# Kernel tuning notes

Measured on AMD Instinct MI355X. Metric: run time of the kernel, lower is better.

## Reference

```python
import jax, jax.numpy as jnp
import numpy as np
import math

# Model/config constants (from LunarisCodexConfig defaults)
B, S, D = 4, 4096, 768
E = 8            # n_experts
TOP_K = 2
H = 2048         # SwiGLU hidden: multiple_of*ceil((2/3*4*768)/256)
CAP_F = 1.25     # capacity_factor
EPS = 1e-6       # RMSNorm eps
ALPHA = 1.0      # 1/sqrt(n_reasoning_steps), n_reasoning_steps=1


def setup_inputs() -> dict:
    key = jax.random.key(0)
    k0, k1, k2, k3 = jax.random.split(key, 4)
    x = jax.random.normal(k0, (B, S, D), jnp.float32)
    gate_w = jax.random.normal(k1, (E, D), jnp.float32) * 0.02          # router
    w13 = jax.random.normal(k2, (E, 2 * H, D), jnp.float32) * 0.02      # fused gate/up per expert
    w2 = jax.random.normal(k3, (E, D, H), jnp.float32) * 0.02           # down proj per expert
    norm_w = jnp.ones((E, D), jnp.float32)                              # per-expert RMSNorm weight
    return {"x": x, "gate_w": gate_w, "w13": w13, "w2": w2, "norm_w": norm_w}


def reference(x, gate_w, w13, w2, norm_w):
    Bx, Sx, Dx = x.shape
    N = Bx * Sx
    cap = int(math.ceil(CAP_F * TOP_K * N / E))
    xf = x.reshape(N, Dx)

    # ---- router in fp32, top-k gating with renormalized weights ----
    logits = xf.astype(jnp.float32) @ gate_w.T                 # [N, E]
    probs = jax.nn.softmax(logits, axis=-1)
    top_p, top_i = jax.lax.top_k(probs, TOP_K)                 # [N, K]
    w = top_p / jnp.sum(top_p, axis=-1, keepdims=True)         # [N, K]

    # ---- vectorized capacity-based dispatch (token-major, k-minor order) ----
    flat_e = top_i.reshape(-1)                                  # [N*K]
    onehot = jax.nn.one_hot(flat_e, E, dtype=jnp.int32)         # [N*K, E]
    pos = jnp.take_along_axis(jnp.cumsum(onehot, axis=0) - 1,
                              flat_e[:, None], axis=1)[:, 0]    # rank within expert
    keep = pos < cap                                            # capacity mask
    didx = flat_e * cap + jnp.minimum(pos, cap - 1)             # slot id in [0, E*cap)
    safe = jnp.where(keep, didx, E * cap)                       # dropped -> scratch row

    x_rep = jnp.repeat(xf, TOP_K, axis=0)                       # [N*K, D]
    buf = jnp.zeros((E * cap + 1, Dx), x.dtype).at[safe].set(x_rep)
    buf = buf[:-1].reshape(E, cap, Dx)                          # [E, C, D]

    z = 2.0 * buf
    z = z * jax.lax.rsqrt(jnp.mean(z * z, axis=-1, keepdims=True) + EPS)
    z = z * norm_w[:, None, :]
    gu = jnp.einsum('ecd,ehd->ech', z, w13)                     # [E, C, 2H]
    g, u = jnp.split(gu, 2, axis=-1)
    y = buf + ALPHA * jnp.einsum('ech,edh->ecd', jax.nn.silu(g) * u, w2)

    # ---- combine: gather back, weight, drop over-capacity slots ----
    y_tok = y.reshape(E * cap, Dx)[didx]                        # [N*K, D]
    cw = (w.reshape(-1) * keep.astype(w.dtype)).astype(x.dtype)
    out = (cw[:, None] * y_tok).reshape(N, TOP_K, Dx).sum(axis=1)
    return out.reshape(Bx, Sx, Dx)
```

## Files before the change

### kernel.cpp

```cpp
#include <hip/hip_runtime.h>
#include <hip/hip_bf16.h>
#include <stdint.h>


#define N_TOK 16384
#define D_    768
#define E_    8
#define H_    2048
#define CAP   5120
#define NK    (N_TOK * 2)
#define EPS_  1e-6f
#define LDE   72

typedef unsigned short u16;
typedef __attribute__((ext_vector_type(8))) __bf16 v8bf;
typedef __attribute__((ext_vector_type(4))) float  v4f;

typedef __attribute__((address_space(3))) unsigned int lds_u32;
typedef const __attribute__((address_space(1))) unsigned int glb_u32;

__device__ __forceinline__ void gload16(const void* g, void* lds) {
    __builtin_amdgcn_global_load_lds((glb_u32*)g, (lds_u32*)lds, 16, 0, 0);
}

__device__ __forceinline__ float bf2f(u16 u) {
    union { uint32_t i; float f; } v; v.i = ((uint32_t)u) << 16; return v.f;
}
__device__ __forceinline__ u16 f2bf(float f) {
    union { uint32_t i; float f; } v; v.f = f;
    uint32_t r = v.i + 0x7fffu + ((v.i >> 16) & 1u);
    return (u16)(r >> 16);
}

__global__ __launch_bounds__(256) void conv_bf16_kernel(
    const float* __restrict__ src, u16* __restrict__ dst, int n4)
{
    for (int i = blockIdx.x * 256 + threadIdx.x; i < n4; i += gridDim.x * 256) {
        float4 v = ((const float4*)src)[i];
        ushort4 o;
        o.x = f2bf(v.x); o.y = f2bf(v.y); o.z = f2bf(v.z); o.w = f2bf(v.w);
        ((ushort4*)dst)[i] = o;
    }
}

__global__ __launch_bounds__(256) void router_kernel(
    const float* __restrict__ x, const float* __restrict__ gate_w,
    int* __restrict__ routerEx, float* __restrict__ routerW)
{
    __shared__ float gw[E_ * D_];
    int t = threadIdx.x;
    for (int i = t; i < E_ * D_; i += 256) gw[i] = gate_w[i];
    __syncthreads();
    int wv = t >> 6, l = t & 63;
    int n = blockIdx.x * 4 + wv;
    const float* xr = x + (size_t)n * D_;
    float p[E_];
#pragma unroll
    for (int e = 0; e < E_; ++e) p[e] = 0.f;
#pragma unroll
    for (int j = 0; j < 12; ++j) {
        int d = l + 64 * j;
        float xv = xr[d];
#pragma unroll
        for (int e = 0; e < E_; ++e) p[e] += xv * gw[e * D_ + d];
    }
#pragma unroll
    for (int off = 32; off > 0; off >>= 1) {
#pragma unroll
        for (int e = 0; e < E_; ++e) p[e] += __shfl_xor(p[e], off, 64);
    }
    if (l == 0) {
        int e0 = 0; float m0 = p[0];
#pragma unroll
        for (int e = 1; e < E_; ++e) if (p[e] > m0) { m0 = p[e]; e0 = e; }
        int e1 = (e0 == 0) ? 1 : 0; float m1 = p[e1];
#pragma unroll
        for (int e = 0; e < E_; ++e) if (e != e0 && p[e] > m1) { m1 = p[e]; e1 = e; }
        float w0 = 1.f / (1.f + __expf(m1 - m0));
        routerEx[2 * n] = e0; routerEx[2 * n + 1] = e1;
        routerW[2 * n] = w0; routerW[2 * n + 1] = 1.f - w0;
    }
}

__global__ __launch_bounds__(256) void dispatch_kernel(
    const int* __restrict__ routerEx, int* __restrict__ tokenSlot,
    int* __restrict__ slotToken, int* __restrict__ cnt)
{
    __shared__ int hist[256 * E_];
    int t = threadIdx.x;
    int loc[E_];
#pragma unroll
    for (int e = 0; e < E_; ++e) loc[e] = 0;
    int base = t * (NK / 256);
    for (int j = 0; j < NK / 256; ++j) {
        int ev = routerEx[base + j];
#pragma unroll
        for (int e = 0; e < E_; ++e) loc[e] += (ev == e) ? 1 : 0;
    }
#pragma unroll
    for (int e = 0; e < E_; ++e) hist[t * E_ + e] = loc[e];
    __syncthreads();
    if (t < E_) {
        int run = 0;
        for (int tt = 0; tt < 256; ++tt) { int v = hist[tt * E_ + t]; hist[tt * E_ + t] = run; run += v; }
        cnt[t] = run;
    }
    __syncthreads();
    int off[E_];
#pragma unroll
    for (int e = 0; e < E_; ++e) off[e] = hist[t * E_ + e];
    for (int j = 0; j < NK / 256; ++j) {
        int i = base + j;
        int ev = routerEx[i];
        int pos = 0;
#pragma unroll
        for (int e = 0; e < E_; ++e) { if (ev == e) { pos = off[e]; off[e] = pos + 1; } }
        if (pos < CAP) {
            int s = ev * CAP + pos;
            tokenSlot[i] = s;
            slotToken[s] = i;
        } else {
            tokenSlot[i] = -1;
        }
    }
}

__global__ __launch_bounds__(256) void init_out_kernel(
    const float* __restrict__ x, const int* __restrict__ tokenSlot,
    const float* __restrict__ routerW, float* __restrict__ out)
{
    int g = blockIdx.x * 256 + threadIdx.x;
    int n = g / 96;
    int d0 = (g - n * 96) * 8;
    float w0 = (tokenSlot[2 * n] >= 0) ? routerW[2 * n] : 0.f;
    float w1 = (tokenSlot[2 * n + 1] >= 0) ? routerW[2 * n + 1] : 0.f;
    float ws = w0 + w1;
    const float* xr = x + (size_t)n * D_ + d0;
    float* orow = out + (size_t)n * D_ + d0;
    float4 a = *(const float4*)&xr[0];
    float4 b = *(const float4*)&xr[4];
    float4 oa, ob;
    oa.x = ws * a.x; oa.y = ws * a.y; oa.z = ws * a.z; oa.w = ws * a.w;
    ob.x = ws * b.x; ob.y = ws * b.y; ob.z = ws * b.z; ob.w = ws * b.w;
    *(float4*)&orow[0] = oa;
    *(float4*)&orow[4] = ob;
}

__global__ __launch_bounds__(256) void gather_norm_kernel(
    const float* __restrict__ x, const float* __restrict__ norm_w,
    const int* __restrict__ slotToken, const int* __restrict__ cnt,
    u16* __restrict__ zAll, size_t zStride, int eFixed)
{
    int e = eFixed + blockIdx.z;
    u16* zE = zAll + (size_t)blockIdx.z * zStride;
    int t = threadIdx.x, wv = t >> 6, l = t & 63;
    int pos = blockIdx.x * 4 + wv;
    int ce = min(cnt[e], CAP);
    u16* zr = zE + (size_t)pos * D_;
    if (pos >= ce) {
        ushort4 zz = { 0, 0, 0, 0 };
#pragma unroll
        for (int j = 0; j < 3; ++j) *(ushort4*)&zr[l * 4 + 256 * j] = zz;
        return;
    }
    int tok = slotToken[e * CAP + pos] >> 1;
    const float* xr = x + (size_t)tok * D_;
    float xv[12]; float ss = 0.f;
#pragma unroll
    for (int j = 0; j < 3; ++j) {
        float4 v4 = *(const float4*)&xr[l * 4 + 256 * j];
        xv[4 * j] = v4.x; xv[4 * j + 1] = v4.y; xv[4 * j + 2] = v4.z; xv[4 * j + 3] = v4.w;
        ss += v4.x * v4.x + v4.y * v4.y + v4.z * v4.z + v4.w * v4.w;
    }
#pragma unroll
    for (int off = 32; off > 0; off >>= 1) ss += __shfl_xor(ss, off, 64);
    float rs = rsqrtf(4.f * ss * (1.f / (float)D_) + EPS_);
    const float* nw = norm_w + e * D_;
#pragma unroll
    for (int j = 0; j < 3; ++j) {
        int d0 = l * 4 + 256 * j;
        float4 nv = *(const float4*)&nw[d0];
        ushort4 o;
        o.x = f2bf(2.f * xv[4 * j]     * rs * nv.x);
        o.y = f2bf(2.f * xv[4 * j + 1] * rs * nv.y);
        o.z = f2bf(2.f * xv[4 * j + 2] * rs * nv.z);
        o.w = f2bf(2.f * xv[4 * j + 3] * rs * nv.w);
        *(ushort4*)&zr[d0] = o;
    }
}

__global__ __launch_bounds__(256, 2) void gemm1_kernel(
    const u16* __restrict__ zAll, size_t zStride,
    const u16* __restrict__ w13All, size_t wStride,
    u16* __restrict__ actAll, size_t actStride,
    const int* __restrict__ cnt, int eFixed)
{
    int hw  = blockIdx.y * 32 + blockIdx.x;
    int xcd = hw & 7, cid = hw >> 3;
    int jn  = (xcd & 3) * 8 + (cid & 7);
    int rb  = (xcd >> 2) * 20 + (cid >> 3);
    int e   = eFixed + blockIdx.z;
    int ce  = min(cnt[e], CAP);
    if (rb * 128 >= ce) return;
    const u16* zE   = zAll   + (size_t)blockIdx.z * zStride;
    const u16* w13e = w13All + (size_t)blockIdx.z * wStride;
    u16*       actE = actAll + (size_t)blockIdx.z * actStride;

    __shared__ __align__(16) u16 smem[2 * 128 * 64];
    u16* As = smem;
    u16* Bs = smem + 128 * 64;

    int t = threadIdx.x, w = t >> 6, l = t & 63;
    int lr  = l >> 3;
    int lsw = ((l & 7) ^ lr) << 4;

    const char* aSrc = (const char*)zE
        + (size_t)(rb * 128 + w * 32 + lr) * (D_ * 2) + lsw;
    int rr0   = w * 32 + lr;
    int grow0 = (w < 2) ? (jn * 64 + rr0) : (H_ + jn * 64 + rr0 - 64);
    const char* bSrc = (const char*)w13e + (size_t)grow0 * (D_ * 2) + lsw;

    const v4f vzero = { 0.f, 0.f, 0.f, 0.f };
    v4f acc[2][8];
#pragma unroll
    for (int i = 0; i < 2; ++i)
#pragma unroll
        for (int j = 0; j < 8; ++j) acc[i][j] = vzero;

    int fr = l & 15;
    int sw = (l & 7) << 4;
    int fq = (l >> 4) << 4;

    for (int kb = 0; kb < D_ / 64; ++kb) {
        __syncthreads();
#pragma unroll
        for (int i = 0; i < 4; ++i) {
            gload16(aSrc + i * (8 * D_ * 2), &As[(w * 32 + i * 8) * 64]);
            gload16(bSrc + i * (8 * D_ * 2), &Bs[(w * 32 + i * 8) * 64]);
        }
        aSrc += 128; bSrc += 128;
        __syncthreads();
#pragma unroll
        for (int ks = 0; ks < 2; ++ks) {
            int kby = (ks * 64 + fq) ^ sw;
            v8bf a0 = *(const v8bf*)((const char*)As + (w * 32      + fr) * 128 + kby);
            v8bf a1 = *(const v8bf*)((const char*)As + (w * 32 + 16 + fr) * 128 + kby);
            v8bf bv[8];
#pragma unroll
            for (int ct = 0; ct < 8; ++ct)
                bv[ct] = *(const v8bf*)((const char*)Bs + (ct * 16 + fr) * 128 + kby);
#pragma unroll
            for (int ct = 0; ct < 8; ++ct) {
                acc[0][ct] = __builtin_amdgcn_mfma_f32_16x16x32_bf16(a0, bv[ct], acc[0][ct], 0, 0, 0);
                acc[1][ct] = __builtin_amdgcn_mfma_f32_16x16x32_bf16(a1, bv[ct], acc[1][ct], 0, 0, 0);
            }
        }
    }
    __syncthreads();
    u16* ep = smem;
    int colb = l & 15, rowq = (l >> 4) * 4;
#pragma unroll
    for (int rt = 0; rt < 2; ++rt) {
#pragma unroll
        for (int cg = 0; cg < 4; ++cg) {
            v4f g = acc[rt][cg], u = acc[rt][cg + 4];
#pragma unroll
            for (int r = 0; r < 4; ++r) {
                int rl = w * 32 + rt * 16 + rowq + r;
                float gv = g[r], uv = u[r];
                ep[rl * LDE + cg * 16 + colb] = f2bf(gv / (1.f + __expf(-gv)) * uv);
            }
        }
    }
    __syncthreads();
#pragma unroll
    for (int i = 0; i < 4; ++i) {
        int rl = (t >> 3) + 32 * i;
        int c0 = (t & 7) * 8;
        uint4 v = *(const uint4*)&ep[rl * LDE + c0];
        *(uint4*)&actE[(size_t)(rb * 128 + rl) * H_ + jn * 64 + c0] = v;
    }
}

template <bool WRITE_DELTA>
__global__ __launch_bounds__(256, 2) void gemm2_kernel(
    const u16* __restrict__ actAll, size_t actStride,
    const u16* __restrict__ w2All, size_t wStride,
    const int* __restrict__ slotToken, const float* __restrict__ routerW,
    float* __restrict__ out, u16* __restrict__ deltaAll, size_t deltaStride,
    const int* __restrict__ cnt, int eFixed)
{
    int hw  = blockIdx.y * 12 + blockIdx.x;
    int xcd = hw & 7, cid = hw >> 3;
    int jn  = cid % 12;
    int rb  = xcd * 5 + cid / 12;
    int e   = eFixed + blockIdx.z;
    int ce  = min(cnt[e], CAP);
    if (rb * 128 >= ce) return;
    const u16* actE = actAll + (size_t)blockIdx.z * actStride;
    const u16* w2e  = w2All  + (size_t)blockIdx.z * wStride;

    __shared__ __align__(16) u16 smem[128 * 64 + 64 * 64];
    u16* As = smem;
    u16* Bs = smem + 128 * 64;

    int t = threadIdx.x, w = t >> 6, l = t & 63;
    int lr  = l >> 3;
    int lsw = ((l & 7) ^ lr) << 4;

    const char* aSrc = (const char*)actE
        + (size_t)(rb * 128 + w * 32 + lr) * (H_ * 2) + lsw;
    const char* bSrc = (const char*)w2e
        + (size_t)(jn * 64 + w * 16 + lr) * (H_ * 2) + lsw;

    const v4f vzero = { 0.f, 0.f, 0.f, 0.f };
    v4f acc[2][4];
#pragma unroll
    for (int i = 0; i < 2; ++i)
#pragma unroll
        for (int j = 0; j < 4; ++j) acc[i][j] = vzero;

    int fr = l & 15;
    int sw = (l & 7) << 4;
    int fq = (l >> 4) << 4;

    for (int kb = 0; kb < H_ / 64; ++kb) {
        __syncthreads();
#pragma unroll
        for (int i = 0; i < 4; ++i)
            gload16(aSrc + i * (8 * H_ * 2), &As[(w * 32 + i * 8) * 64]);
#pragma unroll
        for (int i = 0; i < 2; ++i)
            gload16(bSrc + i * (8 * H_ * 2), &Bs[(w * 16 + i * 8) * 64]);
        aSrc += 128; bSrc += 128;
        __syncthreads();
#pragma unroll
        for (int ks = 0; ks < 2; ++ks) {
            int kby = (ks * 64 + fq) ^ sw;
            v8bf a0 = *(const v8bf*)((const char*)As + (w * 32      + fr) * 128 + kby);
            v8bf a1 = *(const v8bf*)((const char*)As + (w * 32 + 16 + fr) * 128 + kby);
            v8bf bv[4];
#pragma unroll
            for (int ct = 0; ct < 4; ++ct)
                bv[ct] = *(const v8bf*)((const char*)Bs + (ct * 16 + fr) * 128 + kby);
#pragma unroll
            for (int ct = 0; ct < 4; ++ct) {
                acc[0][ct] = __builtin_amdgcn_mfma_f32_16x16x32_bf16(a0, bv[ct], acc[0][ct], 0, 0, 0);
                acc[1][ct] = __builtin_amdgcn_mfma_f32_16x16x32_bf16(a1, bv[ct], acc[1][ct], 0, 0, 0);
            }
        }
    }
    __syncthreads();
    u16* ep = smem;
    int colb = l & 15, rowq = (l >> 4) * 4;
#pragma unroll
    for (int rt = 0; rt < 2; ++rt) {
#pragma unroll
        for (int ct = 0; ct < 4; ++ct) {
            v4f a = acc[rt][ct];
#pragma unroll
            for (int r = 0; r < 4; ++r) {
                int rl = w * 32 + rt * 16 + rowq + r;
                ep[rl * LDE + ct * 16 + colb] = f2bf(a[r]);
            }
        }
    }
    __syncthreads();
    if (WRITE_DELTA) {
        u16* deltaE = deltaAll + (size_t)blockIdx.z * deltaStride;
#pragma unroll
        for (int i = 0; i < 4; ++i) {
            int rl = (t >> 3) + 32 * i;
            int c0 = (t & 7) * 8;
            uint4 v = *(const uint4*)&ep[rl * LDE + c0];
            *(uint4*)&deltaE[(size_t)(rb * 128 + rl) * D_ + jn * 64 + c0] = v;
        }
    } else {
#pragma unroll
        for (int i = 0; i < 8; ++i) {
            int rl = (t >> 4) + 16 * i;
            int grow = rb * 128 + rl;
            if (grow >= ce) continue;
            int idx = slotToken[e * CAP + grow];
            int tok = idx >> 1;
            float wg = routerW[idx];
            int c = (t & 15) * 4;
            const u16* dr = &ep[rl * LDE + c];
            float* orow = out + (size_t)tok * D_ + jn * 64 + c;
            float4 cur = *(const float4*)orow;
            cur.x += wg * bf2f(dr[0]);
            cur.y += wg * bf2f(dr[1]);
            cur.z += wg * bf2f(dr[2]);
            cur.w += wg * bf2f(dr[3]);
            *(float4*)orow = cur;
        }
    }
}

__global__ __launch_bounds__(256) void combine_kernel(
    const float* __restrict__ x, const u16* __restrict__ deltaBuf,
    const int* __restrict__ tokenSlot, const float* __restrict__ routerW,
    float* __restrict__ out)
{
    int g = blockIdx.x * 256 + threadIdx.x;
    int n = g / 192;
    int d0 = (g - n * 192) * 4;
    int s0 = tokenSlot[2 * n], s1 = tokenSlot[2 * n + 1];
    float w0 = (s0 >= 0) ? routerW[2 * n] : 0.f;
    float w1 = (s1 >= 0) ? routerW[2 * n + 1] : 0.f;
    float ws = w0 + w1;
    float4 xv = *(const float4*)&x[(size_t)n * D_ + d0];
    float4 o;
    o.x = ws * xv.x; o.y = ws * xv.y; o.z = ws * xv.z; o.w = ws * xv.w;
    if (s0 >= 0) {
        ushort4 dv = *(const ushort4*)&deltaBuf[(size_t)s0 * D_ + d0];
        o.x += w0 * bf2f(dv.x); o.y += w0 * bf2f(dv.y);
        o.z += w0 * bf2f(dv.z); o.w += w0 * bf2f(dv.w);
    }
    if (s1 >= 0) {
        ushort4 dv = *(const ushort4*)&deltaBuf[(size_t)s1 * D_ + d0];
        o.x += w1 * bf2f(dv.x); o.y += w1 * bf2f(dv.y);
        o.z += w1 * bf2f(dv.z); o.w += w1 * bf2f(dv.w);
    }
    *(float4*)&out[(size_t)n * D_ + d0] = o;
}

extern "C" void kernel_launch(void* const* d_in, const int* in_sizes, int n_in,
                              void* d_out, int out_size, void* d_ws, size_t ws_size,
                              hipStream_t stream)
{
    (void)in_sizes; (void)n_in; (void)out_size;
    const float* x      = (const float*)d_in[0];
    const float* gate_w = (const float*)d_in[1];
    const float* w13    = (const float*)d_in[2];
    const float* w2     = (const float*)d_in[3];
    const float* norm_w = (const float*)d_in[4];
    float* out = (float*)d_out;

    const size_t zSlice   = (size_t)CAP * D_ * 2;
    const size_t actSlice = (size_t)CAP * H_ * 2;
    const size_t w13Slice = (size_t)2 * H_ * D_ * 2;
    const size_t w2Slice  = (size_t)D_ * H_ * 2;
    const size_t ctrl     = (size_t)NK * 4 * 3 + (size_t)E_ * CAP * 4 + 256;

    char* ws = (char*)d_ws;
    size_t off = 0;
    int*   routerEx  = (int*)(ws + off);   off += (size_t)NK * 4;
    float* routerW   = (float*)(ws + off); off += (size_t)NK * 4;
    int*   tokenSlot = (int*)(ws + off);   off += (size_t)NK * 4;
    int*   slotToken = (int*)(ws + off);   off += (size_t)E_ * CAP * 4;
    int*   cnt       = (int*)(ws + off);   off += 256;

    const size_t bigNeed = ctrl + E_ * (zSlice + actSlice + w13Slice + w2Slice) + E_ * zSlice ;
    bool batched = ws_size >= bigNeed;

    router_kernel<<<N_TOK / 4, 256, 0, stream>>>(x, gate_w, routerEx, routerW);
    dispatch_kernel<<<1, 256, 0, stream>>>(routerEx, tokenSlot, slotToken, cnt);

    if (batched) {
        u16* zBuf     = (u16*)(ws + off); off += E_ * zSlice;
        u16* actBuf   = (u16*)(ws + off); off += E_ * actSlice;
        u16* deltaBuf = (u16*)(ws + off); off += E_ * zSlice;
        u16* w13bf    = (u16*)(ws + off); off += E_ * w13Slice;
        u16* w2bf     = (u16*)(ws + off); off += E_ * w2Slice;

        int n13 = E_ * 2 * H_ * D_ / 4, n2 = E_ * D_ * H_ / 4;
        conv_bf16_kernel<<<(n13 + 255) / 256, 256, 0, stream>>>(w13, w13bf, n13);
        conv_bf16_kernel<<<(n2 + 255) / 256, 256, 0, stream>>>(w2, w2bf, n2);
        gather_norm_kernel<<<dim3(CAP / 4, 1, E_), 256, 0, stream>>>(
            x, norm_w, slotToken, cnt, zBuf, zSlice / 2, 0);
        gemm1_kernel<<<dim3(H_ / 64, CAP / 128, E_), 256, 0, stream>>>(
            zBuf, zSlice / 2, w13bf, w13Slice / 2, actBuf, actSlice / 2, cnt, 0);
        gemm2_kernel<true><<<dim3(D_ / 64, CAP / 128, E_), 256, 0, stream>>>(
            actBuf, actSlice / 2, w2bf, w2Slice / 2, slotToken, routerW,
            out, deltaBuf, zSlice / 2, cnt, 0);
        combine_kernel<<<(N_TOK * (D_ / 4)) / 256, 256, 0, stream>>>(
            x, deltaBuf, tokenSlot, routerW, out);
    } else {
        u16* zE   = (u16*)(ws + off); off += zSlice;
        u16* actE = (u16*)(ws + off); off += actSlice;
        u16* w13e = (u16*)(ws + off); off += w13Slice;
        u16* w2e  = (u16*)(ws + off); off += w2Slice;

        init_out_kernel<<<(N_TOK * (D_ / 8)) / 256, 256, 0, stream>>>(x, tokenSlot, routerW, out);
        int n13 = 2 * H_ * D_ / 4, n2 = D_ * H_ / 4;
        for (int e = 0; e < E_; ++e) {
            conv_bf16_kernel<<<(n13 + 255) / 256, 256, 0, stream>>>(
                w13 + (size_t)e * 2 * H_ * D_, w13e, n13);
            conv_bf16_kernel<<<(n2 + 255) / 256, 256, 0, stream>>>(
                w2 + (size_t)e * D_ * H_, w2e, n2);
            gather_norm_kernel<<<dim3(CAP / 4, 1, 1), 256, 0, stream>>>(
                x, norm_w, slotToken, cnt, zE, 0, e);
            gemm1_kernel<<<dim3(H_ / 64, CAP / 128, 1), 256, 0, stream>>>(
                zE, 0, w13e, 0, actE, 0, cnt, e);
            gemm2_kernel<false><<<dim3(D_ / 64, CAP / 128, 1), 256, 0, stream>>>(
                actE, 0, w2e, 0, slotToken, routerW, out, (u16*)nullptr, 0, cnt, e);
        }
    }
}
```

Before: 764.7 us.

## Widen gemm2 output tile to 128 columns and stage router indices in LDS

The down-projection GEMM now computes 128x128 tiles instead of 128x64, halving the number of column blocks. Each block reuses the activation A-tile across twice as many MFMAs and writes its epilogue in two 64-column halves. Separately, the single-block dispatch kernel first copies expert ids into padded byte-sized shared memory and reads them from there, instead of issuing strided global reads twice. The larger tile doubles accumulator registers and halves grid parallelism, which may reduce occupancy.

```diff
diff --git a/kernel.cpp b/kernel.cpp
--- a/kernel.cpp
+++ b/kernel.cpp
@@ -13,6 +13,7 @@
 #define LDE   72
 
 typedef unsigned short u16;
+typedef unsigned char  u8;
 typedef __attribute__((ext_vector_type(8))) __bf16 v8bf;
 typedef __attribute__((ext_vector_type(4))) float  v4f;
 
@@ -86,14 +87,18 @@
     const int* __restrict__ routerEx, int* __restrict__ tokenSlot,
     int* __restrict__ slotToken, int* __restrict__ cnt)
 {
+    __shared__ u8  exs[NK + NK / 128];
     __shared__ int hist[256 * E_];
     int t = threadIdx.x;
+    for (int i = t; i < NK; i += 256)
+        exs[i + (i >> 7)] = (u8)routerEx[i];
+    __syncthreads();
     int loc[E_];
 #pragma unroll
     for (int e = 0; e < E_; ++e) loc[e] = 0;
-    int base = t * (NK / 256);
+    int abase = t * 129;
     for (int j = 0; j < NK / 256; ++j) {
-        int ev = routerEx[base + j];
+        int ev = exs[abase + j];
 #pragma unroll
         for (int e = 0; e < E_; ++e) loc[e] += (ev == e) ? 1 : 0;
     }
@@ -109,9 +114,10 @@
     int off[E_];
 #pragma unroll
     for (int e = 0; e < E_; ++e) off[e] = hist[t * E_ + e];
+    int base = t * (NK / 256);
     for (int j = 0; j < NK / 256; ++j) {
         int i = base + j;
-        int ev = routerEx[i];
+        int ev = exs[abase + j];
         int pos = 0;
 #pragma unroll
         for (int e = 0; e < E_; ++e) { if (ev == e) { pos = off[e]; off[e] = pos + 1; } }
@@ -217,7 +223,7 @@
     const char* aSrc = (const char*)zE
         + (size_t)(rb * 128 + w * 32 + lr) * (D_ * 2) + lsw;
     int rr0   = w * 32 + lr;
-    int grow0 = (w < 2) ? (jn * 64 + rr0) : (H_ + jn * 64 + rr0 - 64);
+    int grow0 = (w < 2) ? (jn * 64 + rr0) : (H_ + jn * 64 + (rr0 - 64));
     const char* bSrc = (const char*)w13e + (size_t)grow0 * (D_ * 2) + lsw;
 
     const v4f vzero = { 0.f, 0.f, 0.f, 0.f };
@@ -290,17 +296,17 @@
     float* __restrict__ out, u16* __restrict__ deltaAll, size_t deltaStride,
     const int* __restrict__ cnt, int eFixed)
 {
-    int hw  = blockIdx.y * 12 + blockIdx.x;
+    int hw  = blockIdx.y * 6 + blockIdx.x;
     int xcd = hw & 7, cid = hw >> 3;
-    int jn  = cid % 12;
-    int rb  = xcd * 5 + cid / 12;
+    int jn  = cid % 6;
+    int rb  = xcd * 5 + cid / 6;
     int e   = eFixed + blockIdx.z;
     int ce  = min(cnt[e], CAP);
     if (rb * 128 >= ce) return;
     const u16* actE = actAll + (size_t)blockIdx.z * actStride;
     const u16* w2e  = w2All  + (size_t)blockIdx.z * wStride;
 
-    __shared__ __align__(16) u16 smem[128 * 64 + 64 * 64];
+    __shared__ __align__(16) u16 smem[2 * 128 * 64];
     u16* As = smem;
     u16* Bs = smem + 128 * 64;
 
@@ -311,14 +317,14 @@
     const char* aSrc = (const char*)actE
         + (size_t)(rb * 128 + w * 32 + lr) * (H_ * 2) + lsw;
     const char* bSrc = (const char*)w2e
-        + (size_t)(jn * 64 + w * 16 + lr) * (H_ * 2) + lsw;
+        + (size_t)(jn * 128 + w * 32 + lr) * (H_ * 2) + lsw;
 
     const v4f vzero = { 0.f, 0.f, 0.f, 0.f };
-    v4f acc[2][4];
+    v4f acc[2][8];
 #pragma unroll
     for (int i = 0; i < 2; ++i)
 #pragma unroll
-        for (int j = 0; j < 4; ++j) acc[i][j] = vzero;
+        for (int j = 0; j < 8; ++j) acc[i][j] = vzero;
 
     int fr = l & 15;
     int sw = (l & 7) << 4;
@@ -327,11 +333,10 @@
     for (int kb = 0; kb < H_ / 64; ++kb) {
         __syncthreads();
 #pragma unroll
-        for (int i = 0; i < 4; ++i)
+        for (int i = 0; i < 4; ++i) {
             gload16(aSrc + i * (8 * H_ * 2), &As[(w * 32 + i * 8) * 64]);
-#pragma unroll
-        for (int i = 0; i < 2; ++i)
-            gload16(bSrc + i * (8 * H_ * 2), &Bs[(w * 16 + i * 8) * 64]);
+            gload16(bSrc + i * (8 * H_ * 2), &Bs[(w * 32 + i * 8) * 64]);
+        }
         aSrc += 128; bSrc += 128;
         __syncthreads();
 #pragma unroll
@@ -339,60 +344,63 @@
             int kby = (ks * 64 + fq) ^ sw;
             v8bf a0 = *(const v8bf*)((const char*)As + (w * 32      + fr) * 128 + kby);
             v8bf a1 = *(const v8bf*)((const char*)As + (w * 32 + 16 + fr) * 128 + kby);
-            v8bf bv[4];
-#pragma unroll
-            for (int ct = 0; ct < 4; ++ct)
+            v8bf bv[8];
+#pragma unroll
+            for (int ct = 0; ct < 8; ++ct)
                 bv[ct] = *(const v8bf*)((const char*)Bs + (ct * 16 + fr) * 128 + kby);
 #pragma unroll
-            for (int ct = 0; ct < 4; ++ct) {
+            for (int ct = 0; ct < 8; ++ct) {
                 acc[0][ct] = __builtin_amdgcn_mfma_f32_16x16x32_bf16(a0, bv[ct], acc[0][ct], 0, 0, 0);
                 acc[1][ct] = __builtin_amdgcn_mfma_f32_16x16x32_bf16(a1, bv[ct], acc[1][ct], 0, 0, 0);
             }
         }
     }
-    __syncthreads();
     u16* ep = smem;
     int colb = l & 15, rowq = (l >> 4) * 4;
 #pragma unroll
-    for (int rt = 0; rt < 2; ++rt) {
-#pragma unroll
-        for (int ct = 0; ct < 4; ++ct) {
-            v4f a = acc[rt][ct];
-#pragma unroll
-            for (int r = 0; r < 4; ++r) {
-                int rl = w * 32 + rt * 16 + rowq + r;
-                ep[rl * LDE + ct * 16 + colb] = f2bf(a[r]);
+    for (int h = 0; h < 2; ++h) {
+        __syncthreads();
+#pragma unroll
+        for (int rt = 0; rt < 2; ++rt) {
+#pragma unroll
+            for (int cc = 0; cc < 4; ++cc) {
+                v4f a = acc[rt][h * 4 + cc];
+#pragma unroll
+                for (int r = 0; r < 4; ++r) {
+                    int rl = w * 32 + rt * 16 + rowq + r;
+                    ep[rl * LDE + cc * 16 + colb] = f2bf(a[r]);
+                }
             }
         }
-    }
-    __syncthreads();
-    if (WRITE_DELTA) {
-        u16* deltaE = deltaAll + (size_t)blockIdx.z * deltaStride;
-#pragma unroll
-        for (int i = 0; i < 4; ++i) {
-            int rl = (t >> 3) + 32 * i;
-            int c0 = (t & 7) * 8;
-            uint4 v = *(const uint4*)&ep[rl * LDE + c0];
-            *(uint4*)&deltaE[(size_t)(rb * 128 + rl) * D_ + jn * 64 + c0] = v;
-        }
-    } else {
-#pragma unroll
-        for (int i = 0; i < 8; ++i) {
-            int rl = (t >> 4) + 16 * i;
-            int grow = rb * 128 + rl;
-            if (grow >= ce) continue;
-            int idx = slotToken[e * CAP + grow];
-            int tok = idx >> 1;
-            float wg = routerW[idx];
-            int c = (t & 15) * 4;
-            const u16* dr = &ep[rl * LDE + c];
-            float* orow = out + (size_t)tok * D_ + jn * 64 + c;
-            float4 cur = *(const float4*)orow;
-            cur.x += wg * bf2f(dr[0]);
-            cur.y += wg * bf2f(dr[1]);
-            cur.z += wg * bf2f(dr[2]);
-            cur.w += wg * bf2f(dr[3]);
-            *(float4*)orow = cur;
+        __syncthreads();
+        if (WRITE_DELTA) {
+            u16* deltaE = deltaAll + (size_t)blockIdx.z * deltaStride;
+#pragma unroll
+            for (int i = 0; i < 4; ++i) {
+                int rl = (t >> 3) + 32 * i;
+                int c0 = (t & 7) * 8;
+                uint4 v = *(const uint4*)&ep[rl * LDE + c0];
+                *(uint4*)&deltaE[(size_t)(rb * 128 + rl) * D_ + jn * 128 + h * 64 + c0] = v;
+            }
+        } else {
+#pragma unroll
+            for (int i = 0; i < 8; ++i) {
+                int rl = (t >> 4) + 16 * i;
+                int grow = rb * 128 + rl;
+                if (grow >= ce) continue;
+                int idx = slotToken[e * CAP + grow];
+                int tok = idx >> 1;
+                float wg = routerW[idx];
+                int c = (t & 15) * 4;
+                const u16* dr = &ep[rl * LDE + c];
+                float* orow = out + (size_t)tok * D_ + jn * 128 + h * 64 + c;
+                float4 cur = *(const float4*)orow;
+                cur.x += wg * bf2f(dr[0]);
+                cur.y += wg * bf2f(dr[1]);
+                cur.z += wg * bf2f(dr[2]);
+                cur.w += wg * bf2f(dr[3]);
+                *(float4*)orow = cur;
+            }
         }
     }
 }
@@ -471,7 +479,7 @@
             x, norm_w, slotToken, cnt, zBuf, zSlice / 2, 0);
         gemm1_kernel<<<dim3(H_ / 64, CAP / 128, E_), 256, 0, stream>>>(
             zBuf, zSlice / 2, w13bf, w13Slice / 2, actBuf, actSlice / 2, cnt, 0);
-        gemm2_kernel<true><<<dim3(D_ / 64, CAP / 128, E_), 256, 0, stream>>>(
+        gemm2_kernel<true><<<dim3(D_ / 128, CAP / 128, E_), 256, 0, stream>>>(
             actBuf, actSlice / 2, w2bf, w2Slice / 2, slotToken, routerW,
             out, deltaBuf, zSlice / 2, cnt, 0);
         combine_kernel<<<(N_TOK * (D_ / 4)) / 256, 256, 0, stream>>>(
@@ -493,7 +501,7 @@
                 x, norm_w, slotToken, cnt, zE, 0, e);
             gemm1_kernel<<<dim3(H_ / 64, CAP / 128, 1), 256, 0, stream>>>(
                 zE, 0, w13e, 0, actE, 0, cnt, e);
-            gemm2_kernel<false><<<dim3(D_ / 64, CAP / 128, 1), 256, 0, stream>>>(
+            gemm2_kernel<false><<<dim3(D_ / 128, CAP / 128, 1), 256, 0, stream>>>(
                 actE, 0, w2e, 0, slotToken, routerW, out, (u16*)nullptr, 0, cnt, e);
         }
     }
```

Result: faster. 708.1 us (-7.4%).
